# Performance work log

Hardware: AMD Instinct MI355X
Metric: run time of the kernel (lower is better)

Reference implementation:

```python
import jax, jax.numpy as jnp
import numpy as np

H = 32        # num_attention_heads (query heads)
G = 8         # num_query_groups (KV heads)
D = 128       # head_dim
HID = 4096    # hidden_size
THETA = 10000.0


def _rope(x, pos):
    # x: [B, h, S, D]; pos: [S]. Rotate-half (LLaMA) convention.
    half = D // 2
    inv_freq = 1.0 / (THETA ** (jnp.arange(0, half, dtype=jnp.float32) / half))
    ang = pos[:, None].astype(jnp.float32) * inv_freq[None, :]   # [S, half]
    cos = jnp.cos(ang)[None, None]                               # [1,1,S,half]
    sin = jnp.sin(ang)[None, None]
    x1, x2 = x[..., :half], x[..., half:]
    return jnp.concatenate([x1 * cos - x2 * sin, x1 * sin + x2 * cos], axis=-1)


def setup_inputs() -> dict:
    key = jax.random.key(0)
    ks = jax.random.split(key, 9)
    s = 0.02
    return {
        "hidden_states": jax.random.normal(ks[0], (1, 2048, HID), jnp.float32),
        "Wq": jax.random.normal(ks[1], (HID, H * D), jnp.float32) * s,
        "bq": jnp.zeros((H * D,), jnp.float32),
        "Wk": jax.random.normal(ks[2], (HID, G * D), jnp.float32) * s,
        "bk": jnp.zeros((G * D,), jnp.float32),
        "Wv": jax.random.normal(ks[3], (HID, G * D), jnp.float32) * s,
        "bv": jnp.zeros((G * D,), jnp.float32),
        "Wo": jax.random.normal(ks[4], (H * D, HID), jnp.float32) * s,
        "bo": jnp.zeros((HID,), jnp.float32),
    }


def reference(hidden_states, Wq, bq, Wk, bk, Wv, bv, Wo, bo):
    B, S, _ = hidden_states.shape
    R = H // G  # query heads per KV group

    q = hidden_states @ Wq + bq  # [B,S,H*D]
    k = hidden_states @ Wk + bk  # [B,S,G*D]
    v = hidden_states @ Wv + bv  # [B,S,G*D]

    q = q.reshape(B, S, H, D).transpose(0, 2, 1, 3)  # [B,H,S,D]
    k = k.reshape(B, S, G, D).transpose(0, 2, 1, 3)  # [B,G,S,D]
    v = v.reshape(B, S, G, D).transpose(0, 2, 1, 3)  # [B,G,S,D]

    pos = jnp.arange(S)
    q = _rope(q, pos)
    k = _rope(k, pos)

    # Grouped attention: broadcast KV across the R query heads of each group
    qg = q.reshape(B, G, R, S, D)
    scores = jnp.einsum('bgrsd,bgtd->bgrst', qg, k) / jnp.sqrt(jnp.float32(D))
    causal = jnp.tril(jnp.ones((S, S), dtype=bool))
    scores = jnp.where(causal[None, None, None], scores, jnp.finfo(scores.dtype).min)
    probs = jax.nn.softmax(scores, axis=-1)
    ctx = jnp.einsum('bgrst,bgtd->bgrsd', probs, v)          # [B,G,R,S,D]
    ctx = ctx.reshape(B, H, S, D).transpose(0, 2, 1, 3).reshape(B, S, H * D)
    return ctx @ Wo + bo
```

## Files before the change

### kernel.cpp

```cpp
#include <hip/hip_runtime.h>
#include <hip/hip_bf16.h>
#include <math.h>

#define HID   4096
#define NH    32
#define NG    8
#define DH    128
#define SEQ   2048
#define QKV_N 6144
#define KOFF  4096
#define VOFF  5120

typedef __bf16 bf16x8 __attribute__((ext_vector_type(8)));
typedef float  f32x4  __attribute__((ext_vector_type(4)));
using bf16 = __hip_bfloat16;

#define LOG2E 1.4426950408889634f
#define SCALE 0.08838834764831845f

typedef const __attribute__((address_space(1))) void* gas_p;
typedef __attribute__((address_space(3))) void* las_p;
__device__ __forceinline__ void async_copy16(void* lds, const void* g) {
  __builtin_amdgcn_global_load_lds((gas_p)g, (las_p)lds, 16, 0, 0);
}

__device__ __forceinline__ unsigned pack2(float a, float b) {
  union { bf16 h[2]; unsigned u; } t;
  t.h[0] = __float2bfloat16(a);
  t.h[1] = __float2bfloat16(b);
  return t.u;
}

__global__ void cast_x_kernel(const float* __restrict__ x, bf16* __restrict__ y, int n4) {
  int i = blockIdx.x * blockDim.x + threadIdx.x;
  if (i >= n4) return;
  float4 v = ((const float4*)x)[i];
  union { bf16 h[4]; uint2 u; } t;
  t.h[0] = __float2bfloat16(v.x);
  t.h[1] = __float2bfloat16(v.y);
  t.h[2] = __float2bfloat16(v.z);
  t.h[3] = __float2bfloat16(v.w);
  ((uint2*)y)[i] = t.u;
}

__global__ __launch_bounds__(256) void wtrans_all_kernel(const float* __restrict__ Wq, const float* __restrict__ Wk,
                                                         const float* __restrict__ Wv, const float* __restrict__ Wo,
                                                         bf16* __restrict__ Wqkv_t, bf16* __restrict__ Wot) {
  __shared__ bf16 T[64][72];
  const int bx = blockIdx.x;
  const float* W; bf16* dst; int N, ntile;
  if (bx < 64)      { W = Wq; dst = Wqkv_t;                      N = 4096; ntile = bx; }
  else if (bx < 80) { W = Wk; dst = Wqkv_t + (size_t)KOFF * HID; N = 1024; ntile = bx - 64; }
  else if (bx < 96) { W = Wv; dst = Wqkv_t + (size_t)VOFF * HID; N = 1024; ntile = bx - 80; }
  else              { W = Wo; dst = Wot;                         N = 4096; ntile = bx - 96; }
  const int n0 = ntile * 64, k0 = blockIdx.y * 64;
  const int t = threadIdx.x;
  const int nn = (t & 15) * 4, kk = t >> 4;
#pragma unroll
  for (int p = 0; p < 4; ++p) {
    const int k = kk + p * 16;
    float4 v = *(const float4*)&W[(size_t)(k0 + k) * N + n0 + nn];
    union { bf16 h[4]; uint2 u; } c;
    c.h[0] = __float2bfloat16(v.x);
    c.h[1] = __float2bfloat16(v.y);
    c.h[2] = __float2bfloat16(v.z);
    c.h[3] = __float2bfloat16(v.w);
    *(uint2*)&T[k][nn] = c.u;
  }
  __syncthreads();
  const int kc = t & 7, nr = t >> 3;
#pragma unroll
  for (int p = 0; p < 2; ++p) {
    const int n = nr + p * 32;
    union { bf16 h[8]; uint4 u; } o;
#pragma unroll
    for (int i = 0; i < 8; ++i) o.h[i] = T[kc * 8 + i][n];
    *(uint4*)&dst[(size_t)(n0 + n) * HID + k0 + kc * 8] = o.u;
  }
}

__global__ void bias_concat_kernel(const float* __restrict__ bq, const float* __restrict__ bk,
                                   const float* __restrict__ bv, float* __restrict__ dst) {
  int i = blockIdx.x * blockDim.x + threadIdx.x;
  if (i < 4096)       dst[i] = bq[i];
  else if (i < 5120)  dst[i] = bk[i - 4096];
  else if (i < 6144)  dst[i] = bv[i - 5120];
}

__device__ __forceinline__ void st_out(float* C, size_t idx, float v) { C[idx] = v; }
__device__ __forceinline__ void st_out(bf16*  C, size_t idx, float v) { C[idx] = __float2bfloat16(v); }

template <typename OutT>
__global__ __launch_bounds__(256) void gemm_bt_kernel(const bf16* __restrict__ A, const bf16* __restrict__ Bt,
                                                      const float* __restrict__ bias, OutT* __restrict__ C,
                                                      int M, int N, int K) {
  __shared__ alignas(16) bf16 As[128][32];
  __shared__ alignas(16) bf16 Bs[128][32];
  const int tid = threadIdx.x;
  const int w = tid >> 6, lane = tid & 63, quad = lane >> 4, l16 = lane & 15;
  const int wr = w >> 1, wc = w & 1;
  const int m0 = blockIdx.y * 128, n0 = blockIdx.x * 128;
  const int srow = lane >> 2;
  const int scol = (lane & 3) * 8;

  f32x4 acc[4][4];
  f32x4 zero4 = {0.f, 0.f, 0.f, 0.f};
#pragma unroll
  for (int mt = 0; mt < 4; ++mt)
#pragma unroll
    for (int nt = 0; nt < 4; ++nt) acc[mt][nt] = zero4;

  const int nIter = K >> 5;
  for (int kb = 0; kb < nIter; ++kb) {
    const int k0 = kb << 5;
#pragma unroll
    for (int c = 0; c < 2; ++c) {
      const int rb = w * 16 + c * 64;
      async_copy16(&As[rb][0], A  + (size_t)(m0 + rb + srow) * K + k0 + scol);
      async_copy16(&Bs[rb][0], Bt + (size_t)(n0 + rb + srow) * K + k0 + scol);
    }
    __syncthreads();
    bf16x8 af[4], bfr[4];
#pragma unroll
    for (int i = 0; i < 4; ++i) {
      af[i]  = *(const bf16x8*)&As[wr * 64 + i * 16 + l16][quad * 8];
      bfr[i] = *(const bf16x8*)&Bs[wc * 64 + i * 16 + l16][quad * 8];
    }
#pragma unroll
    for (int mt = 0; mt < 4; ++mt)
#pragma unroll
      for (int nt = 0; nt < 4; ++nt)
        acc[mt][nt] = __builtin_amdgcn_mfma_f32_16x16x32_bf16(af[mt], bfr[nt], acc[mt][nt], 0, 0, 0);
    __syncthreads();
  }

#pragma unroll
  for (int nt = 0; nt < 4; ++nt) {
    const int col = n0 + wc * 64 + nt * 16 + l16;
    const float bv = bias[col];
#pragma unroll
    for (int mt = 0; mt < 4; ++mt) {
#pragma unroll
      for (int r = 0; r < 4; ++r) {
        const int row = m0 + wr * 64 + mt * 16 + quad * 4 + r;
        st_out(C, (size_t)row * N + col, acc[mt][nt][r] + bv);
      }
    }
  }
}

__global__ __launch_bounds__(256) void rope_vtrans_kernel(bf16* __restrict__ qkv, bf16* __restrict__ vt) {
  __shared__ bf16 tle[32][33];
  const int bx = blockIdx.x;
  const int tid = threadIdx.x;
  if (bx < 2560) {
    int t = bx * 256 + tid;
    int c  = t & 7;
    int hs = (t >> 3) % 40;
    int s  = t / 320;
    int base = (hs < 32) ? hs * 128 : KOFF + (hs - 32) * 128;
    bf16* p = qkv + (size_t)s * QKV_N + base + c * 8;
    union { bf16x8 v; bf16 h[8]; } a, b, ra, rb;
    a.v = *(bf16x8*)p;
    b.v = *(bf16x8*)(p + 64);
#pragma unroll
    for (int j = 0; j < 8; ++j) {
      int d = c * 8 + j;
      float inv = expf(d * -0.14391156862f);
      float ang = (float)s * inv;
      float sn, cs;
      sincosf(ang, &sn, &cs);
      float x1 = __bfloat162float(a.h[j]);
      float x2 = __bfloat162float(b.h[j]);
      ra.h[j] = __float2bfloat16(x1 * cs - x2 * sn);
      rb.h[j] = __float2bfloat16(x1 * sn + x2 * cs);
    }
    *(bf16x8*)p        = ra.v;
    *(bf16x8*)(p + 64) = rb.v;
  } else {
    const int b = bx - 2560;
    const int s0 = (b & 63) * 32, d0 = ((b >> 6) & 3) * 32, g = b >> 8;
    const int tx = tid & 31, ty = tid >> 5;
#pragma unroll
    for (int i = 0; i < 4; ++i)
      tle[ty + i * 8][tx] = qkv[(size_t)(s0 + ty + i * 8) * QKV_N + VOFF + g * 128 + d0 + tx];
    __syncthreads();
#pragma unroll
    for (int i = 0; i < 4; ++i)
      vt[(size_t)(g * 128 + d0 + ty + i * 8) * SEQ + s0 + tx] = tle[tx][ty + i * 8];
  }
}

__global__ __launch_bounds__(256, 2) void attn_kernel(const bf16* __restrict__ qkv, const bf16* __restrict__ vt,
                                                      bf16* __restrict__ ctx) {
  __shared__ bf16 Ks[2][64][128];
  __shared__ bf16 Vs[2][128][64];

  const int bx = blockIdx.x;
  const int h  = blockIdx.y;
  const int g  = h >> 2;
  const int tid = threadIdx.x, w = tid >> 6, lane = tid & 63;
  const int quad = lane >> 4, l16 = lane & 15;
  const int sw = l16 & 7;

  const float c1 = SCALE * LOG2E;
  const float c2 = 12.0f * LOG2E;

  const int addrA = (((quad & 1) << 5) + l16) * 4;
  const int addrB = addrA + 64;
  const bool hiq = quad >= 2;

  f32x4 zero4 = {0.f, 0.f, 0.f, 0.f};

  auto stage = [&](int kt2, int buf) {
    const bf16* kg = qkv + (size_t)(kt2 * 64) * QKV_N + KOFF + g * 128;
    const bf16* vg = vt + (size_t)(g * 128) * SEQ + kt2 * 64;
#pragma unroll
    for (int i = 0; i < 4; ++i) {
      const int c = (i * 4 + w) * 64 + lane;
      {
        const int key = c >> 4, j = c & 15;
        const int js = (j & 8) | ((j ^ key) & 7);
        async_copy16(&Ks[buf][0][0] + (size_t)(i * 4 + w) * 512,
                     kg + (size_t)key * QKV_N + js * 8);
      }
      {
        const int d = c >> 3, k8 = c & 7;
        const int js = (k8 ^ d) & 7;
        async_copy16(&Vs[buf][0][0] + (size_t)(i * 4 + w) * 512,
                     vg + (size_t)d * SEQ + js * 8);
      }
    }
  };

  for (int ph = 0; ph < 2; ++ph) {
    const int qt = ph ? bx : (31 - bx);
    const int n  = qt + 1;

    bf16x8 qf[4];
    {
      const int qrow = qt * 64 + w * 16 + l16;
      const bf16* qp = qkv + (size_t)qrow * QKV_N + h * 128 + quad * 8;
#pragma unroll
      for (int ks = 0; ks < 4; ++ks) qf[ks] = *(const bf16x8*)(qp + ks * 32);
    }

    f32x4 o[8];
#pragma unroll
    for (int dt = 0; dt < 8; ++dt) o[dt] = zero4;
    float rsum = 0.f;

    __syncthreads();
    stage(0, 0);

    for (int kt = 0; kt < n; ++kt) {
      const int cur = kt & 1;
      __syncthreads();
      if (kt + 1 < n) stage(kt + 1, 1 - cur);

      f32x4 s[4];
#pragma unroll
      for (int nt = 0; nt < 4; ++nt) {
        s[nt] = zero4;
#pragma unroll
        for (int ks = 0; ks < 4; ++ks) {
          const int ch = ks * 4 + quad;
          bf16x8 kf = *(const bf16x8*)&Ks[cur][nt * 16 + l16][((ch & 8) | ((ch ^ l16) & 7)) * 8];
          s[nt] = __builtin_amdgcn_mfma_f32_16x16x32_bf16(kf, qf[ks], s[nt], 0, 0, 0);
        }
      }

#pragma unroll
      for (int nt = 0; nt < 4; ++nt)
#pragma unroll
        for (int r = 0; r < 4; ++r)
          s[nt][r] = exp2f(fmaf(s[nt][r], c1, -c2));

      if (kt == qt) {
        const int q_local = w * 16 + l16;
#pragma unroll
        for (int nt = 0; nt < 4; ++nt)
#pragma unroll
          for (int r = 0; r < 4; ++r)
            if (nt * 16 + quad * 4 + r > q_local) s[nt][r] = 0.f;
      }

#pragma unroll
      for (int nt = 0; nt < 4; ++nt)
        rsum += (s[nt][0] + s[nt][1]) + (s[nt][2] + s[nt][3]);

      unsigned pk[4][2];
#pragma unroll
      for (int nt = 0; nt < 4; ++nt) {
        pk[nt][0] = pack2(s[nt][0], s[nt][1]);
        pk[nt][1] = pack2(s[nt][2], s[nt][3]);
      }

#pragma unroll
      for (int k2 = 0; k2 < 2; ++k2) {
        const int lo = 2 * k2, hi = lo + 1;
        int a0l = __builtin_amdgcn_ds_bpermute(addrA, (int)pk[lo][0]);
        int a1l = __builtin_amdgcn_ds_bpermute(addrA, (int)pk[lo][1]);
        int b0l = __builtin_amdgcn_ds_bpermute(addrB, (int)pk[lo][0]);
        int b1l = __builtin_amdgcn_ds_bpermute(addrB, (int)pk[lo][1]);
        int a0h = __builtin_amdgcn_ds_bpermute(addrA, (int)pk[hi][0]);
        int a1h = __builtin_amdgcn_ds_bpermute(addrA, (int)pk[hi][1]);
        int b0h = __builtin_amdgcn_ds_bpermute(addrB, (int)pk[hi][0]);
        int b1h = __builtin_amdgcn_ds_bpermute(addrB, (int)pk[hi][1]);
        union { int u[4]; bf16x8 v; } pf;
        pf.u[0] = hiq ? a0h : a0l;
        pf.u[1] = hiq ? a1h : a1l;
        pf.u[2] = hiq ? b0h : b0l;
        pf.u[3] = hiq ? b1h : b1l;
#pragma unroll
        for (int dt = 0; dt < 8; ++dt) {
          const int ch = k2 * 4 + quad;
          bf16x8 vf = *(const bf16x8*)&Vs[cur][dt * 16 + l16][((ch ^ sw) & 7) * 8];
          o[dt] = __builtin_amdgcn_mfma_f32_16x16x32_bf16(vf, pf.v, o[dt], 0, 0, 0);
        }
      }
    }

    rsum += __shfl_xor(rsum, 16, 64);
    rsum += __shfl_xor(rsum, 32, 64);
    const float inv = 1.0f / rsum;
    const int srow = qt * 64 + w * 16 + l16;
    bf16* cp = ctx + (size_t)srow * HID + h * 128 + quad * 4;
#pragma unroll
    for (int dt = 0; dt < 8; ++dt) {
      union { bf16 h[4]; uint2 u; } ov;
#pragma unroll
      for (int r = 0; r < 4; ++r) ov.h[r] = __float2bfloat16(o[dt][r] * inv);
      *(uint2*)(cp + dt * 16) = ov.u;
    }
  }
}

extern "C" void kernel_launch(void* const* d_in, const int* in_sizes, int n_in,
                              void* d_out, int out_size, void* d_ws, size_t ws_size,
                              hipStream_t stream) {
  const float* X  = (const float*)d_in[0];
  const float* Wq = (const float*)d_in[1];
  const float* bq = (const float*)d_in[2];
  const float* Wk = (const float*)d_in[3];
  const float* bk = (const float*)d_in[4];
  const float* Wv = (const float*)d_in[5];
  const float* bv = (const float*)d_in[6];
  const float* Wo = (const float*)d_in[7];
  const float* bo = (const float*)d_in[8];
  float* out = (float*)d_out;

  char* ws = (char*)d_ws;
  size_t off = 0;
  auto alloc = [&](size_t bytes) { char* p = ws + off; off += (bytes + 255) & ~255ULL; return p; };
  bf16*  Xb     = (bf16*) alloc((size_t)SEQ * HID * 2);
  bf16*  Wqkv_t = (bf16*) alloc((size_t)QKV_N * HID * 2);
  bf16*  Wot    = (bf16*) alloc((size_t)HID * HID * 2);
  float* bqkv   = (float*)alloc((size_t)QKV_N * 4);
  bf16*  QKV    = (bf16*) alloc((size_t)SEQ * QKV_N * 2);
  bf16*  Vt     = (bf16*) alloc((size_t)NG * DH * SEQ * 2);
  bf16*  Ctx    = (bf16*) alloc((size_t)SEQ * HID * 2);

  cast_x_kernel<<<SEQ * HID / 4 / 256, 256, 0, stream>>>(X, Xb, SEQ * HID / 4);
  wtrans_all_kernel<<<dim3(160, HID / 64), 256, 0, stream>>>(Wq, Wk, Wv, Wo, Wqkv_t, Wot);
  bias_concat_kernel<<<QKV_N / 256, 256, 0, stream>>>(bq, bk, bv, bqkv);

  gemm_bt_kernel<bf16><<<dim3(QKV_N / 128, SEQ / 128), 256, 0, stream>>>(Xb, Wqkv_t, bqkv, QKV, SEQ, QKV_N, HID);
  rope_vtrans_kernel<<<2560 + 2048, 256, 0, stream>>>(QKV, Vt);
  attn_kernel<<<dim3(16, NH), 256, 0, stream>>>(QKV, Vt, Ctx);
  gemm_bt_kernel<float><<<dim3(HID / 128, SEQ / 128), 256, 0, stream>>>(Ctx, Wot, bo, out, SEQ, HID, HID);
}
```

Before: 547.6 us.

## Split attention key tile across waves and reduce partial outputs in LDS

Each wave now handles a 16-key slice of the key tile for all 64 query rows, instead of all 64 keys for its own 16 query rows. This removes the ds_bpermute shuffles used to rearrange P into an MFMA operand; P now goes straight into the MFMA with half the K operand zero-padded. The cost is four times as many output accumulators per wave (o[4][8]) and an LDS cross-wave reduction of partial outputs and row sums at the end. That adds register pressure, wastes half of each PV MFMA, and adds extra syncs. The GEMM kernel also switches to precomputed, incrementing load pointers in place of per-iteration address math.

After: 636.0 us. 1.16x slower.

```diff
diff --git a/kernel.cpp b/kernel.cpp
--- a/kernel.cpp
+++ b/kernel.cpp
@@ -103,6 +103,16 @@
   const int srow = lane >> 2;
   const int scol = (lane & 3) * 8;
 
+  const size_t step64 = (size_t)64 * K;
+  const bf16* pa0 = A  + (size_t)(m0 + w * 16 + srow) * K + scol;
+  const bf16* pa1 = pa0 + step64;
+  const bf16* pb0 = Bt + (size_t)(n0 + w * 16 + srow) * K + scol;
+  const bf16* pb1 = pb0 + step64;
+  bf16* const la0 = &As[w * 16][0];
+  bf16* const la1 = &As[w * 16 + 64][0];
+  bf16* const lb0 = &Bs[w * 16][0];
+  bf16* const lb1 = &Bs[w * 16 + 64][0];
+
   f32x4 acc[4][4];
   f32x4 zero4 = {0.f, 0.f, 0.f, 0.f};
 #pragma unroll
@@ -112,13 +122,11 @@
 
   const int nIter = K >> 5;
   for (int kb = 0; kb < nIter; ++kb) {
-    const int k0 = kb << 5;
-#pragma unroll
-    for (int c = 0; c < 2; ++c) {
-      const int rb = w * 16 + c * 64;
-      async_copy16(&As[rb][0], A  + (size_t)(m0 + rb + srow) * K + k0 + scol);
-      async_copy16(&Bs[rb][0], Bt + (size_t)(n0 + rb + srow) * K + k0 + scol);
-    }
+    async_copy16(la0, pa0);
+    async_copy16(la1, pa1);
+    async_copy16(lb0, pb0);
+    async_copy16(lb1, pb1);
+    pa0 += 32; pa1 += 32; pb0 += 32; pb1 += 32;
     __syncthreads();
     bf16x8 af[4], bfr[4];
 #pragma unroll
@@ -193,22 +201,19 @@
 
 __global__ __launch_bounds__(256, 2) void attn_kernel(const bf16* __restrict__ qkv, const bf16* __restrict__ vt,
                                                       bf16* __restrict__ ctx) {
-  __shared__ bf16 Ks[2][64][128];
-  __shared__ bf16 Vs[2][128][64];
+  __shared__ alignas(16) bf16 Ks[2][64][128];
+  __shared__ alignas(16) bf16 Vs[2][128][64];
+  __shared__ float rsbuf[4][16];
+  float* const red = (float*)&Ks[0][0][0];
 
   const int bx = blockIdx.x;
   const int h  = blockIdx.y;
   const int g  = h >> 2;
   const int tid = threadIdx.x, w = tid >> 6, lane = tid & 63;
   const int quad = lane >> 4, l16 = lane & 15;
-  const int sw = l16 & 7;
 
   const float c1 = SCALE * LOG2E;
   const float c2 = 12.0f * LOG2E;
-
-  const int addrA = (((quad & 1) << 5) + l16) * 4;
-  const int addrB = addrA + 64;
-  const bool hiq = quad >= 2;
 
   f32x4 zero4 = {0.f, 0.f, 0.f, 0.f};
 
@@ -237,18 +242,20 @@
     const int qt = ph ? bx : (31 - bx);
     const int n  = qt + 1;
 
-    bf16x8 qf[4];
-    {
-      const int qrow = qt * 64 + w * 16 + l16;
-      const bf16* qp = qkv + (size_t)qrow * QKV_N + h * 128 + quad * 8;
-#pragma unroll
-      for (int ks = 0; ks < 4; ++ks) qf[ks] = *(const bf16x8*)(qp + ks * 32);
-    }
-
-    f32x4 o[8];
-#pragma unroll
-    for (int dt = 0; dt < 8; ++dt) o[dt] = zero4;
-    float rsum = 0.f;
+    bf16x8 qf[4][4];
+#pragma unroll
+    for (int t = 0; t < 4; ++t) {
+      const bf16* qp = qkv + (size_t)(qt * 64 + t * 16 + l16) * QKV_N + h * 128 + quad * 8;
+#pragma unroll
+      for (int ks = 0; ks < 4; ++ks) qf[t][ks] = *(const bf16x8*)(qp + ks * 32);
+    }
+
+    f32x4 o[4][8];
+#pragma unroll
+    for (int t = 0; t < 4; ++t)
+#pragma unroll
+      for (int dt = 0; dt < 8; ++dt) o[t][dt] = zero4;
+    float rsum[4] = {0.f, 0.f, 0.f, 0.f};
 
     __syncthreads();
     stage(0, 0);
@@ -258,80 +265,92 @@
       __syncthreads();
       if (kt + 1 < n) stage(kt + 1, 1 - cur);
 
+      bf16x8 kf[4];
+#pragma unroll
+      for (int ks = 0; ks < 4; ++ks) {
+        const int ch = ks * 4 + quad;
+        kf[ks] = *(const bf16x8*)&Ks[cur][w * 16 + l16][((ch & 8) | ((ch ^ l16) & 7)) * 8];
+      }
       f32x4 s[4];
 #pragma unroll
-      for (int nt = 0; nt < 4; ++nt) {
-        s[nt] = zero4;
-#pragma unroll
-        for (int ks = 0; ks < 4; ++ks) {
-          const int ch = ks * 4 + quad;
-          bf16x8 kf = *(const bf16x8*)&Ks[cur][nt * 16 + l16][((ch & 8) | ((ch ^ l16) & 7)) * 8];
-          s[nt] = __builtin_amdgcn_mfma_f32_16x16x32_bf16(kf, qf[ks], s[nt], 0, 0, 0);
-        }
-      }
-
-#pragma unroll
-      for (int nt = 0; nt < 4; ++nt)
+      for (int t = 0; t < 4; ++t) {
+        s[t] = zero4;
+#pragma unroll
+        for (int ks = 0; ks < 4; ++ks)
+          s[t] = __builtin_amdgcn_mfma_f32_16x16x32_bf16(kf[ks], qf[t][ks], s[t], 0, 0, 0);
+      }
+
+#pragma unroll
+      for (int t = 0; t < 4; ++t)
 #pragma unroll
         for (int r = 0; r < 4; ++r)
-          s[nt][r] = exp2f(fmaf(s[nt][r], c1, -c2));
+          s[t][r] = exp2f(fmaf(s[t][r], c1, -c2));
 
       if (kt == qt) {
-        const int q_local = w * 16 + l16;
-#pragma unroll
-        for (int nt = 0; nt < 4; ++nt)
+        const int keyl = w * 16 + quad * 4;
+#pragma unroll
+        for (int t = 0; t < 4; ++t)
 #pragma unroll
           for (int r = 0; r < 4; ++r)
-            if (nt * 16 + quad * 4 + r > q_local) s[nt][r] = 0.f;
-      }
-
-#pragma unroll
-      for (int nt = 0; nt < 4; ++nt)
-        rsum += (s[nt][0] + s[nt][1]) + (s[nt][2] + s[nt][3]);
-
-      unsigned pk[4][2];
-#pragma unroll
-      for (int nt = 0; nt < 4; ++nt) {
-        pk[nt][0] = pack2(s[nt][0], s[nt][1]);
-        pk[nt][1] = pack2(s[nt][2], s[nt][3]);
-      }
-
-#pragma unroll
-      for (int k2 = 0; k2 < 2; ++k2) {
-        const int lo = 2 * k2, hi = lo + 1;
-        int a0l = __builtin_amdgcn_ds_bpermute(addrA, (int)pk[lo][0]);
-        int a1l = __builtin_amdgcn_ds_bpermute(addrA, (int)pk[lo][1]);
-        int b0l = __builtin_amdgcn_ds_bpermute(addrB, (int)pk[lo][0]);
-        int b1l = __builtin_amdgcn_ds_bpermute(addrB, (int)pk[lo][1]);
-        int a0h = __builtin_amdgcn_ds_bpermute(addrA, (int)pk[hi][0]);
-        int a1h = __builtin_amdgcn_ds_bpermute(addrA, (int)pk[hi][1]);
-        int b0h = __builtin_amdgcn_ds_bpermute(addrB, (int)pk[hi][0]);
-        int b1h = __builtin_amdgcn_ds_bpermute(addrB, (int)pk[hi][1]);
-        union { int u[4]; bf16x8 v; } pf;
-        pf.u[0] = hiq ? a0h : a0l;
-        pf.u[1] = hiq ? a1h : a1l;
-        pf.u[2] = hiq ? b0h : b0l;
-        pf.u[3] = hiq ? b1h : b1l;
-#pragma unroll
-        for (int dt = 0; dt < 8; ++dt) {
-          const int ch = k2 * 4 + quad;
-          bf16x8 vf = *(const bf16x8*)&Vs[cur][dt * 16 + l16][((ch ^ sw) & 7) * 8];
-          o[dt] = __builtin_amdgcn_mfma_f32_16x16x32_bf16(vf, pf.v, o[dt], 0, 0, 0);
-        }
-      }
-    }
-
-    rsum += __shfl_xor(rsum, 16, 64);
-    rsum += __shfl_xor(rsum, 32, 64);
-    const float inv = 1.0f / rsum;
-    const int srow = qt * 64 + w * 16 + l16;
-    bf16* cp = ctx + (size_t)srow * HID + h * 128 + quad * 4;
-#pragma unroll
-    for (int dt = 0; dt < 8; ++dt) {
-      union { bf16 h[4]; uint2 u; } ov;
-#pragma unroll
-      for (int r = 0; r < 4; ++r) ov.h[r] = __float2bfloat16(o[dt][r] * inv);
-      *(uint2*)(cp + dt * 16) = ov.u;
+            if (keyl + r > t * 16 + l16) s[t][r] = 0.f;
+      }
+
+#pragma unroll
+      for (int t = 0; t < 4; ++t)
+        rsum[t] += (s[t][0] + s[t][1]) + (s[t][2] + s[t][3]);
+
+      union { unsigned u[4]; bf16x8 v; } pf[4];
+#pragma unroll
+      for (int t = 0; t < 4; ++t) {
+        pf[t].u[0] = pack2(s[t][0], s[t][1]);
+        pf[t].u[1] = pack2(s[t][2], s[t][3]);
+        pf[t].u[2] = 0;
+        pf[t].u[3] = 0;
+      }
+
+      const int vch = ((w * 2 + (quad >> 1)) ^ (l16 & 7)) * 8 + (quad & 1) * 4;
+#pragma unroll
+      for (int dt = 0; dt < 8; ++dt) {
+        union { unsigned u[4]; bf16x8 v; } af;
+        *(uint2*)&af.u[0] = *(const uint2*)&Vs[cur][dt * 16 + l16][vch];
+        af.u[2] = 0;
+        af.u[3] = 0;
+#pragma unroll
+        for (int t = 0; t < 4; ++t)
+          o[t][dt] = __builtin_amdgcn_mfma_f32_16x16x32_bf16(af.v, pf[t].v, o[t][dt], 0, 0, 0);
+      }
+    }
+
+    float rst[4];
+#pragma unroll
+    for (int t = 0; t < 4; ++t) {
+      float v = rsum[t];
+      v += __shfl_xor(v, 16, 64);
+      v += __shfl_xor(v, 32, 64);
+      rst[t] = v;
+    }
+#pragma unroll
+    for (int t = 0; t < 4; ++t) {
+      __syncthreads();
+#pragma unroll
+      for (int dt = 0; dt < 8; ++dt)
+        *(f32x4*)&red[(((w * 8 + dt) * 64) + lane) * 4] = o[t][dt];
+      if (quad == 0) rsbuf[w][l16] = rst[t];
+      __syncthreads();
+#pragma unroll
+      for (int i = 0; i < 2; ++i) {
+        const int dt = w * 2 + i;
+        f32x4 a0 = *(const f32x4*)&red[(((0 * 8 + dt) * 64) + lane) * 4];
+        f32x4 a1 = *(const f32x4*)&red[(((1 * 8 + dt) * 64) + lane) * 4];
+        f32x4 a2 = *(const f32x4*)&red[(((2 * 8 + dt) * 64) + lane) * 4];
+        f32x4 a3 = *(const f32x4*)&red[(((3 * 8 + dt) * 64) + lane) * 4];
+        f32x4 sum = (a0 + a1) + (a2 + a3);
+        const float inv = 1.0f / (rsbuf[0][l16] + rsbuf[1][l16] + rsbuf[2][l16] + rsbuf[3][l16]);
+        union { bf16 hh[4]; uint2 u; } ov;
+#pragma unroll
+        for (int r = 0; r < 4; ++r) ov.hh[r] = __float2bfloat16(sum[r] * inv);
+        *(uint2*)&ctx[(size_t)(qt * 64 + t * 16 + l16) * HID + h * 128 + dt * 16 + quad * 4] = ov.u;
+      }
     }
   }
 }
```
